# Optimization experiments

Measured on AMD Instinct MI355X. Metric: run time of the kernel, lower is better.

## Reference

```python
import jax, jax.numpy as jnp
import numpy as np
from jax import lax

DIM = 96
HEADS = 3
EPS = 1e-12


def conv1x1(x, w):
    # x: [b,c,h,w], w: [o,c]
    return jnp.einsum('bchw,oc->bohw', x, w)


def dwconv3(x, w):
    # depthwise 3x3, SAME padding. w: [C,1,3,3]
    C = x.shape[1]
    return lax.conv_general_dilated(
        x, w, window_strides=(1, 1), padding='SAME',
        feature_group_count=C,
        dimension_numbers=('NCHW', 'OIHW', 'NCHW'))


def channel_attn(q, kv, temperature):
    # q: [b,C,h,w], kv: [b,2C,h,w], temperature: [heads,1,1]
    k, v = jnp.split(kv, 2, axis=1)
    b, C, h, w = q.shape
    c = C // HEADS
    r = lambda x: x.reshape(b, HEADS, c, h * w)
    q, k, v = r(q), r(k), r(v)
    # L2-normalize along the (h*w) axis (torch F.normalize semantics)
    qn = q / jnp.maximum(jnp.linalg.norm(q, axis=-1, keepdims=True), EPS)
    kn = k / jnp.maximum(jnp.linalg.norm(k, axis=-1, keepdims=True), EPS)
    attn = jnp.einsum('bhcn,bhdn->bhcd', qn, kn) * temperature  # [b,heads,c,c]
    attn = jax.nn.softmax(attn, axis=-1)
    out = jnp.einsum('bhcd,bhdn->bhcn', attn, v)
    return out.reshape(b, C, h, w)


def setup_inputs() -> dict:
    key = jax.random.key(0)
    ks = jax.random.split(key, 16)
    d = DIM
    s = lambda fan: 1.0 / np.sqrt(fan)
    inp = {
        'low': jax.random.normal(ks[0], (2, d, 256, 256), jnp.float32),
        'high': jax.random.normal(ks[1], (2, d, 256, 256), jnp.float32),
        'temperature': jnp.ones((HEADS, 1, 1), jnp.float32),
        'qc_w': jax.random.normal(ks[2], (d, d), jnp.float32) * s(d),
        'qdw_c_w': jax.random.normal(ks[3], (d, 1, 3, 3), jnp.float32) * s(9),
        'kvc_w': jax.random.normal(ks[4], (2 * d, d), jnp.float32) * s(d),
        'kvdw_c_w': jax.random.normal(ks[5], (2 * d, 1, 3, 3), jnp.float32) * s(9),
        'qt_w': jax.random.normal(ks[6], (d, d), jnp.float32) * s(d),
        'qdw_t_w': jax.random.normal(ks[7], (d, 1, 3, 3), jnp.float32) * s(9),
        'kvt_w': jax.random.normal(ks[8], (2 * d, d), jnp.float32) * s(d),
        'kvdw_t_w': jax.random.normal(ks[9], (2 * d, 1, 3, 3), jnp.float32) * s(9),
        'po_c_w': jax.random.normal(ks[10], (d, d), jnp.float32) * s(d),
        'po_t_w': jax.random.normal(ks[11], (d, d), jnp.float32) * s(d),
        'concat_w': jax.random.normal(ks[12], (d, 2 * d), jnp.float32) * s(2 * d),
        'concat_b': jax.random.normal(ks[13], (d,), jnp.float32) * s(2 * d),
    }
    return inp


def reference(low, high, temperature, qc_w, qdw_c_w, kvc_w, kvdw_c_w,
              qt_w, qdw_t_w, kvt_w, kvdw_t_w, po_c_w, po_t_w,
              concat_w, concat_b):
    q_c = dwconv3(conv1x1(high, qc_w), qdw_c_w)
    kv_c = dwconv3(conv1x1(high, kvc_w), kvdw_c_w)
    q_t = dwconv3(conv1x1(low, qt_w), qdw_t_w)
    kv_t = dwconv3(conv1x1(low, kvt_w), kvdw_t_w)
    out_c = conv1x1(channel_attn(q_c, kv_t, temperature), po_c_w)
    out_t = conv1x1(channel_attn(q_t, kv_c, temperature), po_t_w)
    out = jnp.concatenate([out_c, out_t], axis=1)
    out = conv1x1(out, concat_w) + concat_b[None, :, None, None]
    return out
```

## Files before the change

kernel.cpp:

```cpp
#include <hip/hip_runtime.h>
#include <hip/hip_bf16.h>

#define HW 65536
#define GNS 64

typedef __attribute__((ext_vector_type(8))) short short8;
typedef __attribute__((ext_vector_type(4))) float f32x4;
union U8 { short8 s; unsigned u[4]; ushort h[8]; };

static __device__ __forceinline__ ushort f2bf(float f) {
    union { float f; unsigned u; } v; v.f = f;
    unsigned u = v.u;
    unsigned r = (u + 0x7fffu + ((u >> 16) & 1u)) >> 16;
    return (ushort)r;
}
static __device__ __forceinline__ float bf2f(ushort u) {
    union { unsigned u; float f; } v; v.u = ((unsigned)u) << 16; return v.f;
}
static __device__ __forceinline__ unsigned pk2(float a, float b) {
    __hip_bfloat162 h = __float22bfloat162_rn(make_float2(a, b));
    union { __hip_bfloat162 h; unsigned u; } c; c.h = h; return c.u;
}
static __device__ __forceinline__ f32x4 mfma16(short8 a, short8 b, f32x4 c) {
    return __builtin_amdgcn_mfma_f32_16x16x32_bf16(a, b, c, 0, 0, 0);
}

__global__ __launch_bounds__(256) void prep_kernel(
        const float* __restrict__ qc, const float* __restrict__ kvc,
        const float* __restrict__ qt, const float* __restrict__ kvt,
        const float* __restrict__ cw, const float* __restrict__ poc, const float* __restrict__ pot,
        ushort* __restrict__ Wc, ushort* __restrict__ Wt,
        float* __restrict__ W1, float* __restrict__ W2, float* __restrict__ SSQ) {
    int bx = blockIdx.x, tid = threadIdx.x;
    if (bx < 9) {
        for (int idx = bx * 256 + tid; idx < 288 * 96; idx += 9 * 256) {
            Wc[idx] = f2bf(idx < 96 * 96 ? qc[idx] : kvc[idx - 96 * 96]);
            Wt[idx] = f2bf(idx < 96 * 96 ? qt[idx] : kvt[idx - 96 * 96]);
        }
        if (bx == 0)
            for (int idx = tid; idx < 8 * 96; idx += 256) SSQ[idx] = 0.f;
    } else {
        int idx = (bx - 9) * 256 + tid;
        int sel = idx < 9216 ? 0 : 1;
        int i = sel ? idx - 9216 : idx;
        int o = i / 96, m = i % 96;
        const float* po = sel ? pot : poc;
        float acc = 0.f;
        for (int p = 0; p < 96; ++p)
            acc += cw[o * 192 + sel * 96 + p] * po[p * 96 + m];
        (sel ? W2 : W1)[i] = acc;
    }
}

__global__ __launch_bounds__(256, 2) void conv_kernel(const float* __restrict__ X,
                                                      const ushort* __restrict__ W,
                                                      ushort* __restrict__ Y) {
    __shared__ ushort xs[96][136];
    int tid = threadIdx.x;
    int n0 = blockIdx.x * 128;
    int b = blockIdx.y;
    int wave = tid >> 6, lane = tid & 63, lr = lane & 15, lg = lane >> 4;
    const float* Xb = X + (size_t)b * 96 * HW + n0;
    #pragma unroll
    for (int i = 0; i < 12; ++i) {
        int idx = tid + i * 256;
        int ch = idx >> 5, g = idx & 31;
        float4 v = *(const float4*)(Xb + (size_t)ch * HW + 4 * g);
        unsigned* d = (unsigned*)&xs[ch][4 * g];
        d[0] = pk2(v.x, v.y);
        d[1] = pk2(v.z, v.w);
    }
    __syncthreads();
    short8 af[2][3];
    #pragma unroll
    for (int nt = 0; nt < 2; ++nt) {
        int n = wave * 32 + nt * 16 + lr;
        #pragma unroll
        for (int kk = 0; kk < 3; ++kk) {
            int kb = kk * 32 + lg * 8;
            U8 t;
            #pragma unroll
            for (int j = 0; j < 4; ++j) {
                unsigned e0 = xs[kb + 2 * j][n];
                unsigned e1 = xs[kb + 2 * j + 1][n];
                t.u[j] = e0 | (e1 << 16);
            }
            af[nt][kk] = t.s;
        }
    }
    __syncthreads();
    ushort* ys = &xs[0][0];
    int row0 = tid >> 4, g = tid & 15;
    for (int og = 0; og < 3; ++og) {
        const ushort* Wg = W + (size_t)og * 96 * 96 + (size_t)lr * 96 + lg * 8;
        #pragma unroll
        for (int mt = 0; mt < 6; ++mt) {
            f32x4 a0 = {0.f, 0.f, 0.f, 0.f}, a1 = {0.f, 0.f, 0.f, 0.f};
            #pragma unroll
            for (int kk = 0; kk < 3; ++kk) {
                short8 wf = *(const short8*)(Wg + (size_t)mt * 16 * 96 + kk * 32);
                a0 = mfma16(af[0][kk], wf, a0);
                a1 = mfma16(af[1][kk], wf, a1);
            }
            unsigned* d0 = (unsigned*)&ys[(mt * 16 + lr) * 136 + wave * 32 + lg * 4];
            d0[0] = pk2(a0[0], a0[1]);
            d0[1] = pk2(a0[2], a0[3]);
            unsigned* d1 = (unsigned*)&ys[(mt * 16 + lr) * 136 + wave * 32 + 16 + lg * 4];
            d1[0] = pk2(a1[0], a1[1]);
            d1[1] = pk2(a1[2], a1[3]);
        }
        __syncthreads();
        ushort* Yg = Y + (size_t)(b * 288 + og * 96) * HW + n0;
        #pragma unroll
        for (int p = 0; p < 6; ++p) {
            int row = p * 16 + row0;
            *(short8*)&Yg[(size_t)row * HW + 8 * g] = *(const short8*)&ys[row * 136 + 8 * g];
        }
        __syncthreads();
    }
}

__global__ __launch_bounds__(256) void dw_kernel(const ushort* __restrict__ Y,
                                                 const float* __restrict__ qdw,
                                                 const float* __restrict__ kvdw,
                                                 ushort* __restrict__ QKV,
                                                 float* __restrict__ SSQ, int is_c) {
    __shared__ ushort tile[34 * 256];
    int tid = threadIdx.x;
    int ch = blockIdx.y % 288, b = blockIdx.y / 288;
    int r0 = blockIdx.x * 32;
    const float* w = (ch < 96) ? (qdw + ch * 9) : (kvdw + (ch - 96) * 9);
    float w00 = w[0], w01 = w[1], w02 = w[2], w10 = w[3], w11 = w[4],
          w12 = w[5], w20 = w[6], w21 = w[7], w22 = w[8];
    const ushort* src = Y + (size_t)(b * 288 + ch) * HW;
    #pragma unroll
    for (int i = 0; i < 5; ++i) {
        int idx = tid + i * 256;
        if (idx < 34 * 32) {
            int row = idx >> 5, g = idx & 31;
            int gr = r0 - 1 + row;
            short8 v;
            if (gr >= 0 && gr < 256) v = *(const short8*)(src + gr * 256 + 8 * g);
            else v = (short8){0, 0, 0, 0, 0, 0, 0, 0};
            *(short8*)&tile[row * 256 + 8 * g] = v;
        }
    }
    __syncthreads();
    int wave = tid >> 6, lane = tid & 63;
    float rows[3][6];
    float ssq = 0.f;
    #define LOADROW(LROW, D)                                                 \
    {                                                                        \
        ushort4 t4 = *(const ushort4*)&tile[(LROW) * 256 + 4 * lane];        \
        float c0 = bf2f(t4.x), c1 = bf2f(t4.y), c2 = bf2f(t4.z), c3 = bf2f(t4.w); \
        float lft = __shfl(c3, lane - 1);                                    \
        float rgt = __shfl(c0, lane + 1);                                    \
        if (lane == 0) lft = 0.f;                                            \
        if (lane == 63) rgt = 0.f;                                           \
        D[0] = lft; D[1] = c0; D[2] = c1; D[3] = c2; D[4] = c3; D[5] = rgt;  \
    }
    LOADROW(wave * 8 + 0, rows[0]);
    LOADROW(wave * 8 + 1, rows[1]);
    ushort* dst = QKV + (size_t)(b * 288 + ch) * HW;
    #pragma unroll
    for (int orow = 0; orow < 8; ++orow) {
        LOADROW(wave * 8 + orow + 2, rows[(orow + 2) % 3]);
        float* ra = rows[orow % 3];
        float* rb = rows[(orow + 1) % 3];
        float* rc = rows[(orow + 2) % 3];
        float acc[4];
        #pragma unroll
        for (int j = 0; j < 4; ++j) {
            acc[j] = w00 * ra[j] + w01 * ra[j + 1] + w02 * ra[j + 2]
                   + w10 * rb[j] + w11 * rb[j + 1] + w12 * rb[j + 2]
                   + w20 * rc[j] + w21 * rc[j + 1] + w22 * rc[j + 2];
            ssq += acc[j] * acc[j];
        }
        uint2 pv;
        pv.x = pk2(acc[0], acc[1]);
        pv.y = pk2(acc[2], acc[3]);
        *(uint2*)&dst[(r0 + wave * 8 + orow) * 256 + 4 * lane] = pv;
    }
    #undef LOADROW
    if (ch < 192) {
        #pragma unroll
        for (int off = 1; off < 64; off <<= 1) ssq += __shfl_xor(ssq, off);
        if (lane == 0) {
            int t_ = ch >= 96;
            int chq = t_ ? ch - 96 : ch;
            int a_ = is_c ? t_ : (1 - t_);
            atomicAdd(&SSQ[((a_ * 2 + b) * 2 + t_) * 96 + chq], ssq);
        }
    }
}

__global__ __launch_bounds__(256) void gram_kernel(const ushort* __restrict__ QKVc,
                                                   const ushort* __restrict__ QKVt,
                                                   float* __restrict__ Gpart) {
    __shared__ ushort qs[32 * 256];
    __shared__ ushort ks2[32 * 256];
    __shared__ float Gp[4][32][32];
    int tid = threadIdx.x, wave = tid >> 6, lane = tid & 63;
    int lr = lane & 15, lg = lane >> 4;
    int code = blockIdx.y;
    int a = code / 6, b = (code % 6) / 3, h = code % 3;
    const ushort* qsrc = (a == 0) ? QKVc : QKVt;
    const ushort* ksrc = (a == 0) ? QKVt : QKVc;
    const ushort* qb = qsrc + (size_t)(b * 288 + 32 * h) * HW + blockIdx.x * 1024;
    const ushort* kb = ksrc + (size_t)(b * 288 + 96 + 32 * h) * HW + blockIdx.x * 1024;
    f32x4 acc[2][2];
    #pragma unroll
    for (int i = 0; i < 2; ++i)
        #pragma unroll
        for (int j = 0; j < 2; ++j) acc[i][j] = (f32x4){0.f, 0.f, 0.f, 0.f};
    for (int ph = 0; ph < 4; ++ph) {
        int noff = ph * 256;
        #pragma unroll
        for (int i = 0; i < 4; ++i) {
            int idx = tid + i * 256;
            int row = idx >> 5, g = idx & 31;
            int col = (g * 8) ^ ((row & 7) << 3);
            *(short8*)&qs[row * 256 + col] = *(const short8*)(qb + (size_t)row * HW + noff + 8 * g);
            *(short8*)&ks2[row * 256 + col] = *(const short8*)(kb + (size_t)row * HW + noff + 8 * g);
        }
        __syncthreads();
        #pragma unroll
        for (int j = 0; j < 2; ++j) {
            int ks_ = wave * 2 + j;
            int c0 = (ks_ * 32 + lg * 8) ^ ((lr & 7) << 3);
            short8 a0 = *(const short8*)&qs[lr * 256 + c0];
            short8 a1 = *(const short8*)&qs[(16 + lr) * 256 + c0];
            short8 b0 = *(const short8*)&ks2[lr * 256 + c0];
            short8 b1 = *(const short8*)&ks2[(16 + lr) * 256 + c0];
            acc[0][0] = mfma16(a0, b0, acc[0][0]);
            acc[0][1] = mfma16(a0, b1, acc[0][1]);
            acc[1][0] = mfma16(a1, b0, acc[1][0]);
            acc[1][1] = mfma16(a1, b1, acc[1][1]);
        }
        __syncthreads();
    }
    #pragma unroll
    for (int i = 0; i < 2; ++i)
        #pragma unroll
        for (int j = 0; j < 2; ++j)
            #pragma unroll
            for (int r = 0; r < 4; ++r)
                Gp[wave][i * 16 + lg * 4 + r][j * 16 + lr] = acc[i][j][r];
    __syncthreads();
    float* Gout = Gpart + ((size_t)code * GNS + blockIdx.x) * 1024;
    for (int idx = tid; idx < 1024; idx += 256) {
        float ssum = 0.f;
        #pragma unroll
        for (int wv = 0; wv < 4; ++wv) ssum += (&Gp[wv][0][0])[idx];
        Gout[idx] = ssum;
    }
}

__global__ __launch_bounds__(256) void attn_kernel(const float* __restrict__ Gpart,
                                                   const float* __restrict__ SSQ,
                                                   const float* __restrict__ temperature,
                                                   const float* __restrict__ W1,
                                                   const float* __restrict__ W2,
                                                   ushort* __restrict__ Mcat) {
    __shared__ float Gs[1024];
    __shared__ float nq[32], nk[32], A[32][32];
    int tid = threadIdx.x;
    int code = blockIdx.x;
    int a = code / 6, b = (code % 6) / 3, h = code % 3;
    const float* gp = Gpart + (size_t)code * GNS * 1024;
    #pragma unroll
    for (int j = 0; j < 4; ++j) {
        int idx = tid + j * 256;
        float s = 0.f;
        #pragma unroll 8
        for (int p = 0; p < GNS; ++p) s += gp[(size_t)p * 1024 + idx];
        Gs[idx] = s;
    }
    if (tid < 32)
        nq[tid] = fmaxf(sqrtf(fmaxf(SSQ[((a * 2 + b) * 2 + 0) * 96 + 32 * h + tid], 0.f)), 1e-12f);
    else if (tid < 64)
        nk[tid - 32] = fmaxf(sqrtf(fmaxf(SSQ[((a * 2 + b) * 2 + 1) * 96 + 32 * h + (tid - 32)], 0.f)), 1e-12f);
    __syncthreads();
    if (tid < 32) {
        float t = temperature[h];
        float lgv[32];
        float inq = t / nq[tid];
        float mx = -1e30f;
        #pragma unroll
        for (int j = 0; j < 32; ++j) { lgv[j] = Gs[tid * 32 + j] * inq / nk[j]; mx = fmaxf(mx, lgv[j]); }
        float ssum = 0.f;
        #pragma unroll
        for (int j = 0; j < 32; ++j) { lgv[j] = expf(lgv[j] - mx); ssum += lgv[j]; }
        float inv = 1.f / ssum;
        #pragma unroll
        for (int j = 0; j < 32; ++j) A[tid][j] = lgv[j] * inv;
    }
    __syncthreads();
    const float* Wm = (a == 0) ? W1 : W2;
    for (int idx = tid; idx < 96 * 32; idx += 256) {
        int o = idx >> 5, d = idx & 31;
        float acc = 0.f;
        #pragma unroll
        for (int i = 0; i < 32; ++i)
            acc += Wm[o * 96 + 32 * h + i] * A[i][d];
        Mcat[(size_t)(b * 96 + o) * 192 + a * 96 + 32 * h + d] = f2bf(acc);
    }
}

__global__ __launch_bounds__(256, 2) void final_kernel(const ushort* __restrict__ QKVc,
                                                       const ushort* __restrict__ QKVt,
                                                       const ushort* __restrict__ Mcat,
                                                       const float* __restrict__ bias,
                                                       float* __restrict__ out) {
    __shared__ float smem[96 * 132];
    ushort* vs = (ushort*)smem;
    int tid = threadIdx.x;
    int n0 = blockIdx.x * 128, b = blockIdx.y;
    int wave = tid >> 6, lane = tid & 63, lr = lane & 15, lg = lane >> 4;
    #pragma unroll
    for (int i = 0; i < 12; ++i) {
        int idx = tid + i * 256;
        int d = idx >> 4, g = idx & 15;
        const ushort* sp = (d < 96) ? (QKVt + (size_t)(b * 288 + 192 + d) * HW)
                                    : (QKVc + (size_t)(b * 288 + 192 + (d - 96)) * HW);
        U8 t;
        t.s = *(const short8*)(sp + n0 + 8 * g);
        unsigned* dst = (unsigned*)&vs[d * 132 + 8 * g];
        dst[0] = t.u[0]; dst[1] = t.u[1]; dst[2] = t.u[2]; dst[3] = t.u[3];
    }
    __syncthreads();
    short8 vf[2][6];
    #pragma unroll
    for (int nt = 0; nt < 2; ++nt) {
        int n = wave * 32 + nt * 16 + lr;
        #pragma unroll
        for (int kk = 0; kk < 6; ++kk) {
            int kb = kk * 32 + lg * 8;
            U8 t;
            #pragma unroll
            for (int j = 0; j < 4; ++j) {
                unsigned e0 = vs[(kb + 2 * j) * 132 + n];
                unsigned e1 = vs[(kb + 2 * j + 1) * 132 + n];
                t.u[j] = e0 | (e1 << 16);
            }
            vf[nt][kk] = t.s;
        }
    }
    __syncthreads();
    const ushort* Mb = Mcat + (size_t)b * 96 * 192;
    #pragma unroll
    for (int mt = 0; mt < 6; ++mt) {
        f32x4 a0 = {0.f, 0.f, 0.f, 0.f}, a1 = {0.f, 0.f, 0.f, 0.f};
        #pragma unroll
        for (int kk = 0; kk < 6; ++kk) {
            short8 mf = *(const short8*)&Mb[(size_t)(mt * 16 + lr) * 192 + kk * 32 + lg * 8];
            a0 = mfma16(vf[0][kk], mf, a0);
            a1 = mfma16(vf[1][kk], mf, a1);
        }
        *(float4*)&smem[(mt * 16 + lr) * 132 + wave * 32 + lg * 4] =
            make_float4(a0[0], a0[1], a0[2], a0[3]);
        *(float4*)&smem[(mt * 16 + lr) * 132 + wave * 32 + 16 + lg * 4] =
            make_float4(a1[0], a1[1], a1[2], a1[3]);
    }
    __syncthreads();
    float* outb = out + (size_t)b * 96 * HW + n0;
    int row0 = tid >> 5, q = tid & 31;
    #pragma unroll
    for (int p = 0; p < 12; ++p) {
        int row = p * 8 + row0;
        float4 v = *(const float4*)&smem[row * 132 + 4 * q];
        float bb = bias[row];
        v.x += bb; v.y += bb; v.z += bb; v.w += bb;
        *(float4*)&outb[(size_t)row * HW + 4 * q] = v;
    }
}

extern "C" void kernel_launch(void* const* d_in, const int* in_sizes, int n_in,
                              void* d_out, int out_size, void* d_ws, size_t ws_size,
                              hipStream_t stream) {
    const float* low    = (const float*)d_in[0];
    const float* high   = (const float*)d_in[1];
    const float* temp   = (const float*)d_in[2];
    const float* qc_w   = (const float*)d_in[3];
    const float* qdw_c  = (const float*)d_in[4];
    const float* kvc_w  = (const float*)d_in[5];
    const float* kvdw_c = (const float*)d_in[6];
    const float* qt_w   = (const float*)d_in[7];
    const float* qdw_t  = (const float*)d_in[8];
    const float* kvt_w  = (const float*)d_in[9];
    const float* kvdw_t = (const float*)d_in[10];
    const float* po_c   = (const float*)d_in[11];
    const float* po_t   = (const float*)d_in[12];
    const float* cw     = (const float*)d_in[13];
    const float* cb     = (const float*)d_in[14];
    float* out = (float*)d_out;

    char* ws = (char*)d_ws;
    const size_t SY = (size_t)2 * 288 * HW * 2;
    ushort* Y    = (ushort*)(ws);
    ushort* QKVc = (ushort*)(ws + SY);
    ushort* QKVt = (ushort*)(ws + 2 * SY);
    float* Gpart = (float*)ws;
    char* p = ws + 3 * SY;
    ushort* Wc = (ushort*)p; p += 288 * 96 * 2;
    ushort* Wt = (ushort*)p; p += 288 * 96 * 2;
    float* W1  = (float*)p;  p += 96 * 96 * 4;
    float* W2  = (float*)p;  p += 96 * 96 * 4;
    float* SSQ = (float*)p;  p += 8 * 96 * 4;
    ushort* Mcat = (ushort*)p; p += 2 * 96 * 192 * 2;
    if ((size_t)(p - ws) > ws_size) return;

    prep_kernel<<<81, 256, 0, stream>>>(qc_w, kvc_w, qt_w, kvt_w, cw, po_c, po_t, Wc, Wt, W1, W2, SSQ);
    conv_kernel<<<dim3(512, 2), 256, 0, stream>>>(high, Wc, Y);
    dw_kernel<<<dim3(8, 576), 256, 0, stream>>>(Y, qdw_c, kvdw_c, QKVc, SSQ, 1);
    conv_kernel<<<dim3(512, 2), 256, 0, stream>>>(low, Wt, Y);
    dw_kernel<<<dim3(8, 576), 256, 0, stream>>>(Y, qdw_t, kvdw_t, QKVt, SSQ, 0);
    gram_kernel<<<dim3(GNS, 12), 256, 0, stream>>>(QKVc, QKVt, Gpart);
    attn_kernel<<<12, 256, 0, stream>>>(Gpart, SSQ, temp, W1, W2, Mcat);
    final_kernel<<<dim3(512, 2), 256, 0, stream>>>(QKVc, QKVt, Mcat, cb, out);
}
```

Measured before the change: 239.7 us.

## Merge high/low conv and depthwise launches; drop LDS tile in depthwise kernel

Conv and depthwise kernels gain a z grid dimension so both streams (high and low) run in a single launch each when the workspace can hold a fourth buffer. This halves the number of launches and gives each grid more blocks. The depthwise kernel also drops its shared-memory tile and barrier: each wave now reads its rows straight from global memory, with halo rows re-read by neighbouring waves. Its launch bounds are raised to allow more resident blocks. The cost is redundant global/L2 reads for the halo rows and a larger workspace footprint.

```diff
diff --git a/kernel.cpp b/kernel.cpp
--- a/kernel.cpp
+++ b/kernel.cpp
@@ -52,10 +52,15 @@
     }
 }
 
-__global__ __launch_bounds__(256, 2) void conv_kernel(const float* __restrict__ X,
-                                                      const ushort* __restrict__ W,
-                                                      ushort* __restrict__ Y) {
+__global__ __launch_bounds__(256, 2) void conv_kernel(
+        const float* __restrict__ Xc, const float* __restrict__ Xt,
+        const ushort* __restrict__ Wcp, const ushort* __restrict__ Wtp,
+        ushort* __restrict__ Yco, ushort* __restrict__ Yto) {
     __shared__ ushort xs[96][136];
+    int strm = blockIdx.z;
+    const float* X = strm ? Xt : Xc;
+    const ushort* W = strm ? Wtp : Wcp;
+    ushort* Y = strm ? Yto : Yco;
     int tid = threadIdx.x;
     int n0 = blockIdx.x * 128;
     int b = blockIdx.y;
@@ -120,51 +125,47 @@
     }
 }
 
-__global__ __launch_bounds__(256) void dw_kernel(const ushort* __restrict__ Y,
-                                                 const float* __restrict__ qdw,
-                                                 const float* __restrict__ kvdw,
-                                                 ushort* __restrict__ QKV,
-                                                 float* __restrict__ SSQ, int is_c) {
-    __shared__ ushort tile[34 * 256];
-    int tid = threadIdx.x;
+__global__ __launch_bounds__(256, 8) void dw_kernel(
+        const ushort* __restrict__ Yc, const ushort* __restrict__ Yt,
+        const float* __restrict__ qdw_c, const float* __restrict__ kvdw_c,
+        const float* __restrict__ qdw_t, const float* __restrict__ kvdw_t,
+        ushort* __restrict__ QKVc, ushort* __restrict__ QKVt,
+        float* __restrict__ SSQ, int base_strm) {
+    int tid = threadIdx.x, wave = tid >> 6, lane = tid & 63;
+    int strm = base_strm + blockIdx.z;
     int ch = blockIdx.y % 288, b = blockIdx.y / 288;
-    int r0 = blockIdx.x * 32;
+    int r0 = blockIdx.x * 32 + wave * 8;
+    const ushort* Y = strm ? Yt : Yc;
+    ushort* QKV = strm ? QKVt : QKVc;
+    const float* qdw = strm ? qdw_t : qdw_c;
+    const float* kvdw = strm ? kvdw_t : kvdw_c;
     const float* w = (ch < 96) ? (qdw + ch * 9) : (kvdw + (ch - 96) * 9);
     float w00 = w[0], w01 = w[1], w02 = w[2], w10 = w[3], w11 = w[4],
           w12 = w[5], w20 = w[6], w21 = w[7], w22 = w[8];
     const ushort* src = Y + (size_t)(b * 288 + ch) * HW;
-    #pragma unroll
-    for (int i = 0; i < 5; ++i) {
-        int idx = tid + i * 256;
-        if (idx < 34 * 32) {
-            int row = idx >> 5, g = idx & 31;
-            int gr = r0 - 1 + row;
-            short8 v;
-            if (gr >= 0 && gr < 256) v = *(const short8*)(src + gr * 256 + 8 * g);
-            else v = (short8){0, 0, 0, 0, 0, 0, 0, 0};
-            *(short8*)&tile[row * 256 + 8 * g] = v;
-        }
-    }
-    __syncthreads();
-    int wave = tid >> 6, lane = tid & 63;
     float rows[3][6];
     float ssq = 0.f;
-    #define LOADROW(LROW, D)                                                 \
+    #define LOADROW(R, D)                                                    \
     {                                                                        \
-        ushort4 t4 = *(const ushort4*)&tile[(LROW) * 256 + 4 * lane];        \
-        float c0 = bf2f(t4.x), c1 = bf2f(t4.y), c2 = bf2f(t4.z), c3 = bf2f(t4.w); \
-        float lft = __shfl(c3, lane - 1);                                    \
-        float rgt = __shfl(c0, lane + 1);                                    \
-        if (lane == 0) lft = 0.f;                                            \
-        if (lane == 63) rgt = 0.f;                                           \
-        D[0] = lft; D[1] = c0; D[2] = c1; D[3] = c2; D[4] = c3; D[5] = rgt;  \
-    }
-    LOADROW(wave * 8 + 0, rows[0]);
-    LOADROW(wave * 8 + 1, rows[1]);
+        int r_ = (R);                                                        \
+        if ((unsigned)r_ < 256u) {                                           \
+            ushort4 t4 = *(const ushort4*)(src + r_ * 256 + 4 * lane);       \
+            float c0 = bf2f(t4.x), c1 = bf2f(t4.y), c2 = bf2f(t4.z), c3 = bf2f(t4.w); \
+            float lft = __shfl(c3, lane - 1);                                \
+            float rgt = __shfl(c0, lane + 1);                                \
+            if (lane == 0) lft = 0.f;                                        \
+            if (lane == 63) rgt = 0.f;                                       \
+            D[0] = lft; D[1] = c0; D[2] = c1; D[3] = c2; D[4] = c3; D[5] = rgt; \
+        } else {                                                             \
+            D[0] = 0.f; D[1] = 0.f; D[2] = 0.f; D[3] = 0.f; D[4] = 0.f; D[5] = 0.f; \
+        }                                                                    \
+    }
+    LOADROW(r0 - 1, rows[0]);
+    LOADROW(r0, rows[1]);
     ushort* dst = QKV + (size_t)(b * 288 + ch) * HW;
     #pragma unroll
     for (int orow = 0; orow < 8; ++orow) {
-        LOADROW(wave * 8 + orow + 2, rows[(orow + 2) % 3]);
+        LOADROW(r0 + orow + 1, rows[(orow + 2) % 3]);
         float* ra = rows[orow % 3];
         float* rb = rows[(orow + 1) % 3];
         float* rc = rows[(orow + 2) % 3];
@@ -179,7 +180,7 @@
         uint2 pv;
         pv.x = pk2(acc[0], acc[1]);
         pv.y = pk2(acc[2], acc[3]);
-        *(uint2*)&dst[(r0 + wave * 8 + orow) * 256 + 4 * lane] = pv;
+        *(uint2*)&dst[(r0 + orow) * 256 + 4 * lane] = pv;
     }
     #undef LOADROW
     if (ch < 192) {
@@ -188,7 +189,7 @@
         if (lane == 0) {
             int t_ = ch >= 96;
             int chq = t_ ? ch - 96 : ch;
-            int a_ = is_c ? t_ : (1 - t_);
+            int a_ = (strm == 0) ? t_ : (1 - t_);
             atomicAdd(&SSQ[((a_ * 2 + b) * 2 + t_) * 96 + chq], ssq);
         }
     }
@@ -397,11 +398,16 @@
 
     char* ws = (char*)d_ws;
     const size_t SY = (size_t)2 * 288 * HW * 2;
-    ushort* Y    = (ushort*)(ws);
-    ushort* QKVc = (ushort*)(ws + SY);
-    ushort* QKVt = (ushort*)(ws + 2 * SY);
+    const size_t EXTRA = 2 * (size_t)(288 * 96 * 2) + 2 * (size_t)(96 * 96 * 4)
+                       + (size_t)(8 * 96 * 4) + (size_t)(2 * 96 * 192 * 2);
+    bool merged = (ws_size >= 4 * SY + EXTRA);
+    size_t nbig = merged ? 4 : 3;
+    ushort* B0 = (ushort*)(ws);
+    ushort* B1 = (ushort*)(ws + SY);
+    ushort* B2 = (ushort*)(ws + 2 * SY);
+    ushort* B3 = (ushort*)(ws + 3 * SY);
     float* Gpart = (float*)ws;
-    char* p = ws + 3 * SY;
+    char* p = ws + nbig * SY;
     ushort* Wc = (ushort*)p; p += 288 * 96 * 2;
     ushort* Wt = (ushort*)p; p += 288 * 96 * 2;
     float* W1  = (float*)p;  p += 96 * 96 * 4;
@@ -411,10 +417,22 @@
     if ((size_t)(p - ws) > ws_size) return;
 
     prep_kernel<<<81, 256, 0, stream>>>(qc_w, kvc_w, qt_w, kvt_w, cw, po_c, po_t, Wc, Wt, W1, W2, SSQ);
-    conv_kernel<<<dim3(512, 2), 256, 0, stream>>>(high, Wc, Y);
-    dw_kernel<<<dim3(8, 576), 256, 0, stream>>>(Y, qdw_c, kvdw_c, QKVc, SSQ, 1);
-    conv_kernel<<<dim3(512, 2), 256, 0, stream>>>(low, Wt, Y);
-    dw_kernel<<<dim3(8, 576), 256, 0, stream>>>(Y, qdw_t, kvdw_t, QKVt, SSQ, 0);
+    ushort* QKVc;
+    ushort* QKVt;
+    if (merged) {
+        QKVc = B2; QKVt = B3;
+        conv_kernel<<<dim3(512, 2, 2), 256, 0, stream>>>(high, low, Wc, Wt, B0, B1);
+        dw_kernel<<<dim3(8, 576, 2), 256, 0, stream>>>(B0, B1, qdw_c, kvdw_c, qdw_t, kvdw_t,
+                                                       QKVc, QKVt, SSQ, 0);
+    } else {
+        QKVc = B1; QKVt = B2;
+        conv_kernel<<<dim3(512, 2, 1), 256, 0, stream>>>(high, high, Wc, Wc, B0, B0);
+        dw_kernel<<<dim3(8, 576, 1), 256, 0, stream>>>(B0, B0, qdw_c, kvdw_c, qdw_c, kvdw_c,
+                                                       QKVc, QKVc, SSQ, 0);
+        conv_kernel<<<dim3(512, 2, 1), 256, 0, stream>>>(low, low, Wt, Wt, B0, B0);
+        dw_kernel<<<dim3(8, 576, 1), 256, 0, stream>>>(B0, B0, qdw_t, kvdw_t, qdw_t, kvdw_t,
+                                                       QKVt, QKVt, SSQ, 1);
+    }
     gram_kernel<<<dim3(GNS, 12), 256, 0, stream>>>(QKVc, QKVt, Gpart);
     attn_kernel<<<12, 256, 0, stream>>>(Gpart, SSQ, temp, W1, W2, Mcat);
     final_kernel<<<dim3(512, 2), 256, 0, stream>>>(QKVc, QKVt, Mcat, cb, out);
```

Result: faster. 235.0 us (-2.0%).

## Overlap low-stream conv with high-stream depthwise in one merged launch

Applied to the files above, without the earlier changes.

Merges the second 1x1 conv (low input) and the first depthwise conv (high stream) into a single grid so the two independent stages share the GPU concurrently, and rebalances workspace buffers so they do not alias. The depthwise body now reads rows straight from global memory through L1/L2 instead of staging a tile in LDS, allowing higher occupancy. The final kernel processes the 192-wide V in two halves to halve its LDS footprint, and the Gram reduction unroll is increased. Risks include heterogeneous blocks in one launch causing imbalance, and the dw path depending on cache hits for its 3x row reuse.

```diff
diff --git a/kernel.cpp b/kernel.cpp
--- a/kernel.cpp
+++ b/kernel.cpp
@@ -52,13 +52,10 @@
     }
 }
 
-__global__ __launch_bounds__(256, 2) void conv_kernel(const float* __restrict__ X,
-                                                      const ushort* __restrict__ W,
-                                                      ushort* __restrict__ Y) {
-    __shared__ ushort xs[96][136];
-    int tid = threadIdx.x;
-    int n0 = blockIdx.x * 128;
-    int b = blockIdx.y;
+static __device__ __forceinline__ void conv_body(
+        ushort xs[96][136], const float* __restrict__ X,
+        const ushort* __restrict__ W, ushort* __restrict__ Y,
+        int n0, int b, int tid) {
     int wave = tid >> 6, lane = tid & 63, lr = lane & 15, lg = lane >> 4;
     const float* Xb = X + (size_t)b * 96 * HW + n0;
     #pragma unroll
@@ -120,51 +117,40 @@
     }
 }
 
-__global__ __launch_bounds__(256) void dw_kernel(const ushort* __restrict__ Y,
-                                                 const float* __restrict__ qdw,
-                                                 const float* __restrict__ kvdw,
-                                                 ushort* __restrict__ QKV,
-                                                 float* __restrict__ SSQ, int is_c) {
-    __shared__ ushort tile[34 * 256];
-    int tid = threadIdx.x;
-    int ch = blockIdx.y % 288, b = blockIdx.y / 288;
-    int r0 = blockIdx.x * 32;
-    const float* w = (ch < 96) ? (qdw + ch * 9) : (kvdw + (ch - 96) * 9);
-    float w00 = w[0], w01 = w[1], w02 = w[2], w10 = w[3], w11 = w[4],
-          w12 = w[5], w20 = w[6], w21 = w[7], w22 = w[8];
-    const ushort* src = Y + (size_t)(b * 288 + ch) * HW;
-    #pragma unroll
-    for (int i = 0; i < 5; ++i) {
-        int idx = tid + i * 256;
-        if (idx < 34 * 32) {
-            int row = idx >> 5, g = idx & 31;
-            int gr = r0 - 1 + row;
-            short8 v;
-            if (gr >= 0 && gr < 256) v = *(const short8*)(src + gr * 256 + 8 * g);
-            else v = (short8){0, 0, 0, 0, 0, 0, 0, 0};
-            *(short8*)&tile[row * 256 + 8 * g] = v;
-        }
-    }
-    __syncthreads();
-    int wave = tid >> 6, lane = tid & 63;
-    float rows[3][6];
-    float ssq = 0.f;
-    #define LOADROW(LROW, D)                                                 \
-    {                                                                        \
-        ushort4 t4 = *(const ushort4*)&tile[(LROW) * 256 + 4 * lane];        \
+#define DW_LOADROW(R, D)                                                     \
+{                                                                            \
+    int r_ = (R);                                                            \
+    if ((unsigned)r_ < 256u) {                                               \
+        ushort4 t4 = *(const ushort4*)(src + r_ * 256 + 4 * lane);           \
         float c0 = bf2f(t4.x), c1 = bf2f(t4.y), c2 = bf2f(t4.z), c3 = bf2f(t4.w); \
         float lft = __shfl(c3, lane - 1);                                    \
         float rgt = __shfl(c0, lane + 1);                                    \
         if (lane == 0) lft = 0.f;                                            \
         if (lane == 63) rgt = 0.f;                                           \
         D[0] = lft; D[1] = c0; D[2] = c1; D[3] = c2; D[4] = c3; D[5] = rgt;  \
-    }
-    LOADROW(wave * 8 + 0, rows[0]);
-    LOADROW(wave * 8 + 1, rows[1]);
+    } else {                                                                 \
+        D[0] = 0.f; D[1] = 0.f; D[2] = 0.f; D[3] = 0.f; D[4] = 0.f; D[5] = 0.f; \
+    }                                                                        \
+}
+
+static __device__ __forceinline__ void dw_body(
+        const ushort* __restrict__ Y, const float* __restrict__ qdw,
+        const float* __restrict__ kvdw, ushort* __restrict__ QKV,
+        float* __restrict__ SSQ, int strm, int rg, int ch, int b, int tid) {
+    int wave = tid >> 6, lane = tid & 63;
+    int r0 = rg * 32 + wave * 8;
+    const float* w = (ch < 96) ? (qdw + ch * 9) : (kvdw + (ch - 96) * 9);
+    float w00 = w[0], w01 = w[1], w02 = w[2], w10 = w[3], w11 = w[4],
+          w12 = w[5], w20 = w[6], w21 = w[7], w22 = w[8];
+    const ushort* src = Y + (size_t)(b * 288 + ch) * HW;
+    float rows[3][6];
+    float ssq = 0.f;
+    DW_LOADROW(r0 - 1, rows[0]);
+    DW_LOADROW(r0, rows[1]);
     ushort* dst = QKV + (size_t)(b * 288 + ch) * HW;
     #pragma unroll
     for (int orow = 0; orow < 8; ++orow) {
-        LOADROW(wave * 8 + orow + 2, rows[(orow + 2) % 3]);
+        DW_LOADROW(r0 + orow + 1, rows[(orow + 2) % 3]);
         float* ra = rows[orow % 3];
         float* rb = rows[(orow + 1) % 3];
         float* rc = rows[(orow + 2) % 3];
@@ -179,19 +165,50 @@
         uint2 pv;
         pv.x = pk2(acc[0], acc[1]);
         pv.y = pk2(acc[2], acc[3]);
-        *(uint2*)&dst[(r0 + wave * 8 + orow) * 256 + 4 * lane] = pv;
-    }
-    #undef LOADROW
+        *(uint2*)&dst[(r0 + orow) * 256 + 4 * lane] = pv;
+    }
     if (ch < 192) {
         #pragma unroll
         for (int off = 1; off < 64; off <<= 1) ssq += __shfl_xor(ssq, off);
         if (lane == 0) {
             int t_ = ch >= 96;
             int chq = t_ ? ch - 96 : ch;
-            int a_ = is_c ? t_ : (1 - t_);
+            int a_ = (strm == 0) ? t_ : (1 - t_);
             atomicAdd(&SSQ[((a_ * 2 + b) * 2 + t_) * 96 + chq], ssq);
         }
     }
+}
+
+__global__ __launch_bounds__(256, 2) void conv_kernel(const float* __restrict__ X,
+                                                      const ushort* __restrict__ W,
+                                                      ushort* __restrict__ Y) {
+    __shared__ ushort xs[96][136];
+    conv_body(xs, X, W, Y, blockIdx.x * 128, blockIdx.y, threadIdx.x);
+}
+
+__global__ __launch_bounds__(256, 2) void convdw_kernel(
+        const float* __restrict__ Xt, const ushort* __restrict__ Wt,
+        ushort* __restrict__ Yt,
+        const ushort* __restrict__ Yc, const float* __restrict__ qdw_c,
+        const float* __restrict__ kvdw_c, ushort* __restrict__ QKVc,
+        float* __restrict__ SSQ) {
+    __shared__ ushort xs[96][136];
+    int id = blockIdx.x, tid = threadIdx.x;
+    if (id < 1024) {
+        conv_body(xs, Xt, Wt, Yt, (id & 511) * 128, id >> 9, tid);
+    } else {
+        int f = id - 1024;
+        int rg = f & 7, yy = f >> 3;
+        dw_body(Yc, qdw_c, kvdw_c, QKVc, SSQ, 0, rg, yy % 288, yy / 288, tid);
+    }
+}
+
+__global__ __launch_bounds__(256, 8) void dwfull_kernel(
+        const ushort* __restrict__ Y, const float* __restrict__ qdw,
+        const float* __restrict__ kvdw, ushort* __restrict__ QKV,
+        float* __restrict__ SSQ, int strm) {
+    int yy = blockIdx.y;
+    dw_body(Y, qdw, kvdw, QKV, SSQ, strm, blockIdx.x, yy % 288, yy / 288, threadIdx.x);
 }
 
 __global__ __launch_bounds__(256) void gram_kernel(const ushort* __restrict__ QKVc,
@@ -272,7 +289,7 @@
     for (int j = 0; j < 4; ++j) {
         int idx = tid + j * 256;
         float s = 0.f;
-        #pragma unroll 8
+        #pragma unroll 16
         for (int p = 0; p < GNS; ++p) s += gp[(size_t)p * 1024 + idx];
         Gs[idx] = s;
     }
@@ -312,66 +329,82 @@
                                                        const ushort* __restrict__ Mcat,
                                                        const float* __restrict__ bias,
                                                        float* __restrict__ out) {
-    __shared__ float smem[96 * 132];
+    __shared__ float smem[48 * 132];
     ushort* vs = (ushort*)smem;
     int tid = threadIdx.x;
     int n0 = blockIdx.x * 128, b = blockIdx.y;
     int wave = tid >> 6, lane = tid & 63, lr = lane & 15, lg = lane >> 4;
-    #pragma unroll
-    for (int i = 0; i < 12; ++i) {
-        int idx = tid + i * 256;
-        int d = idx >> 4, g = idx & 15;
-        const ushort* sp = (d < 96) ? (QKVt + (size_t)(b * 288 + 192 + d) * HW)
-                                    : (QKVc + (size_t)(b * 288 + 192 + (d - 96)) * HW);
-        U8 t;
-        t.s = *(const short8*)(sp + n0 + 8 * g);
-        unsigned* dst = (unsigned*)&vs[d * 132 + 8 * g];
-        dst[0] = t.u[0]; dst[1] = t.u[1]; dst[2] = t.u[2]; dst[3] = t.u[3];
-    }
-    __syncthreads();
-    short8 vf[2][6];
-    #pragma unroll
-    for (int nt = 0; nt < 2; ++nt) {
-        int n = wave * 32 + nt * 16 + lr;
-        #pragma unroll
-        for (int kk = 0; kk < 6; ++kk) {
-            int kb = kk * 32 + lg * 8;
+    f32x4 acc[6][2];
+    #pragma unroll
+    for (int mt = 0; mt < 6; ++mt) {
+        acc[mt][0] = (f32x4){0.f, 0.f, 0.f, 0.f};
+        acc[mt][1] = (f32x4){0.f, 0.f, 0.f, 0.f};
+    }
+    const ushort* Mb = Mcat + (size_t)b * 96 * 192;
+    for (int half = 0; half < 2; ++half) {
+        #pragma unroll
+        for (int i = 0; i < 6; ++i) {
+            int idx = tid + i * 256;
+            int dl = idx >> 4, g = idx & 15;
+            int d = half * 96 + dl;
+            const ushort* sp = (d < 96) ? (QKVt + (size_t)(b * 288 + 192 + d) * HW)
+                                        : (QKVc + (size_t)(b * 288 + 192 + (d - 96)) * HW);
             U8 t;
+            t.s = *(const short8*)(sp + n0 + 8 * g);
+            unsigned* dst = (unsigned*)&vs[dl * 132 + 8 * g];
+            dst[0] = t.u[0]; dst[1] = t.u[1]; dst[2] = t.u[2]; dst[3] = t.u[3];
+        }
+        __syncthreads();
+        short8 vf[2][3];
+        #pragma unroll
+        for (int nt = 0; nt < 2; ++nt) {
+            int n = wave * 32 + nt * 16 + lr;
             #pragma unroll
-            for (int j = 0; j < 4; ++j) {
-                unsigned e0 = vs[(kb + 2 * j) * 132 + n];
-                unsigned e1 = vs[(kb + 2 * j + 1) * 132 + n];
-                t.u[j] = e0 | (e1 << 16);
+            for (int kk = 0; kk < 3; ++kk) {
+                int kb = kk * 32 + lg * 8;
+                U8 t;
+                #pragma unroll
+                for (int j = 0; j < 4; ++j) {
+                    unsigned e0 = vs[(kb + 2 * j) * 132 + n];
+                    unsigned e1 = vs[(kb + 2 * j + 1) * 132 + n];
+                    t.u[j] = e0 | (e1 << 16);
+                }
+                vf[nt][kk] = t.s;
             }
-            vf[nt][kk] = t.s;
-        }
-    }
-    __syncthreads();
-    const ushort* Mb = Mcat + (size_t)b * 96 * 192;
-    #pragma unroll
-    for (int mt = 0; mt < 6; ++mt) {
-        f32x4 a0 = {0.f, 0.f, 0.f, 0.f}, a1 = {0.f, 0.f, 0.f, 0.f};
-        #pragma unroll
-        for (int kk = 0; kk < 6; ++kk) {
-            short8 mf = *(const short8*)&Mb[(size_t)(mt * 16 + lr) * 192 + kk * 32 + lg * 8];
-            a0 = mfma16(vf[0][kk], mf, a0);
-            a1 = mfma16(vf[1][kk], mf, a1);
-        }
-        *(float4*)&smem[(mt * 16 + lr) * 132 + wave * 32 + lg * 4] =
-            make_float4(a0[0], a0[1], a0[2], a0[3]);
-        *(float4*)&smem[(mt * 16 + lr) * 132 + wave * 32 + 16 + lg * 4] =
-            make_float4(a1[0], a1[1], a1[2], a1[3]);
-    }
-    __syncthreads();
+        }
+        __syncthreads();
+        #pragma unroll
+        for (int mt = 0; mt < 6; ++mt)
+            #pragma unroll
+            for (int kk = 0; kk < 3; ++kk) {
+                short8 mf = *(const short8*)&Mb[(size_t)(mt * 16 + lr) * 192 + half * 96 + kk * 32 + lg * 8];
+                acc[mt][0] = mfma16(vf[0][kk], mf, acc[mt][0]);
+                acc[mt][1] = mfma16(vf[1][kk], mf, acc[mt][1]);
+            }
+    }
     float* outb = out + (size_t)b * 96 * HW + n0;
-    int row0 = tid >> 5, q = tid & 31;
-    #pragma unroll
-    for (int p = 0; p < 12; ++p) {
-        int row = p * 8 + row0;
-        float4 v = *(const float4*)&smem[row * 132 + 4 * q];
-        float bb = bias[row];
-        v.x += bb; v.y += bb; v.z += bb; v.w += bb;
-        *(float4*)&outb[(size_t)row * HW + 4 * q] = v;
+    #pragma unroll
+    for (int half = 0; half < 2; ++half) {
+        #pragma unroll
+        for (int m = 0; m < 3; ++m) {
+            int mt = half * 3 + m;
+            *(float4*)&smem[(m * 16 + lr) * 132 + wave * 32 + lg * 4] =
+                make_float4(acc[mt][0][0], acc[mt][0][1], acc[mt][0][2], acc[mt][0][3]);
+            *(float4*)&smem[(m * 16 + lr) * 132 + wave * 32 + 16 + lg * 4] =
+                make_float4(acc[mt][1][0], acc[mt][1][1], acc[mt][1][2], acc[mt][1][3]);
+        }
+        __syncthreads();
+        #pragma unroll
+        for (int i = 0; i < 6; ++i) {
+            int idx = tid + i * 256;
+            int row = idx >> 5, q = idx & 31;
+            float4 v = *(const float4*)&smem[row * 132 + 4 * q];
+            int grow = half * 48 + row;
+            float bb = bias[grow];
+            v.x += bb; v.y += bb; v.z += bb; v.w += bb;
+            *(float4*)&outb[(size_t)grow * HW + 4 * q] = v;
+        }
+        __syncthreads();
     }
 }
 
@@ -397,10 +430,10 @@
 
     char* ws = (char*)d_ws;
     const size_t SY = (size_t)2 * 288 * HW * 2;
-    ushort* Y    = (ushort*)(ws);
-    ushort* QKVc = (ushort*)(ws + SY);
-    ushort* QKVt = (ushort*)(ws + 2 * SY);
-    float* Gpart = (float*)ws;
+    ushort* B0 = (ushort*)(ws);
+    ushort* B1 = (ushort*)(ws + SY);
+    ushort* B2 = (ushort*)(ws + 2 * SY);
+    float* Gpart = (float*)B1;
     char* p = ws + 3 * SY;
     ushort* Wc = (ushort*)p; p += 288 * 96 * 2;
     ushort* Wt = (ushort*)p; p += 288 * 96 * 2;
@@ -410,11 +443,15 @@
     ushort* Mcat = (ushort*)p; p += 2 * 96 * 192 * 2;
     if ((size_t)(p - ws) > ws_size) return;
 
+    ushort* Yc   = B0;
+    ushort* Yt   = B1;
+    ushort* QKVc = B2;
+    ushort* QKVt = B0;
+
     prep_kernel<<<81, 256, 0, stream>>>(qc_w, kvc_w, qt_w, kvt_w, cw, po_c, po_t, Wc, Wt, W1, W2, SSQ);
-    conv_kernel<<<dim3(512, 2), 256, 0, stream>>>(high, Wc, Y);
-    dw_kernel<<<dim3(8, 576), 256, 0, stream>>>(Y, qdw_c, kvdw_c, QKVc, SSQ, 1);
-    conv_kernel<<<dim3(512, 2), 256, 0, stream>>>(low, Wt, Y);
-    dw_kernel<<<dim3(8, 576), 256, 0, stream>>>(Y, qdw_t, kvdw_t, QKVt, SSQ, 0);
+    conv_kernel<<<dim3(512, 2), 256, 0, stream>>>(high, Wc, Yc);
+    convdw_kernel<<<5632, 256, 0, stream>>>(low, Wt, Yt, Yc, qdw_c, kvdw_c, QKVc, SSQ);
+    dwfull_kernel<<<dim3(8, 576), 256, 0, stream>>>(Yt, qdw_t, kvdw_t, QKVt, SSQ, 1);
     gram_kernel<<<dim3(GNS, 12), 256, 0, stream>>>(QKVc, QKVt, Gpart);
     attn_kernel<<<12, 256, 0, stream>>>(Gpart, SSQ, temp, W1, W2, Mcat);
     final_kernel<<<dim3(512, 2), 256, 0, stream>>>(QKVc, QKVt, Mcat, cb, out);
```

Measured after the change: 225.2 us, median of 2. -6.1%, faster.
